# Kernel tuning notes

Measured on AMD Instinct MI355X. Metric: run time of the kernel, lower is better.

The kernel has to match this reference:

```python
import jax, jax.numpy as jnp
import numpy as np

K = 10

def _lrelu(v):
    return jax.nn.leaky_relu(v, negative_slope=0.2)

def _knn_idx(x, k):
    # x: [B, C, N]; returns indices of k nearest neighbors [B, N, k]
    xx = jnp.sum(x * x, axis=1, keepdims=True)          # [B,1,N]
    inner = -2.0 * jnp.einsum('bcn,bcm->bnm', x, x)     # [B,N,N]
    pd = -xx - inner - jnp.swapaxes(xx, 1, 2)           # -squared distance [B,N,N]
    _, idx = jax.lax.top_k(pd, k)
    return idx

def _graph_feature(x, k):
    # x: [B, C, N] -> edge features [B, 2C, N, k]
    idx = _knn_idx(x, k)                                # [B,N,k]
    xt = jnp.swapaxes(x, 1, 2)                          # [B,N,C]
    feat = jax.vmap(lambda xb, ib: xb[ib])(xt, idx)     # [B,N,k,C] gather
    center = xt[:, :, None, :]                          # [B,N,1,C]
    f = jnp.concatenate([feat - center,
                         jnp.broadcast_to(center, feat.shape)], axis=-1)  # [B,N,k,2C]
    return jnp.transpose(f, (0, 3, 1, 2))               # [B,2C,N,k]

def _edge_block(x, W, k):
    # conv2d 1x1 (no bias) + LeakyReLU + max over neighbors
    g = _graph_feature(x, k)                            # [B,2C,N,k]
    h = _lrelu(jnp.einsum('oc,bcnk->bonk', W, g))
    return jnp.max(h, axis=-1)                          # [B,O,N]

def setup_inputs() -> dict:
    key = jax.random.key(0)
    ks = jax.random.split(key, 9)
    def w(k_, *shape):
        fan_in = shape[-1]
        return jax.random.normal(k_, shape, dtype=jnp.float32) / np.sqrt(fan_in)
    return {
        'x':  jax.random.normal(ks[0], (8, 3, 2048), dtype=jnp.float32),
        'W1': w(ks[1], 64, 6),
        'W2': w(ks[2], 64, 128),
        'W3': w(ks[3], 128, 128),
        'W4': w(ks[4], 256, 256),
        'W5': w(ks[5], 512, 512),
        'L1': w(ks[6], 512, 1024),
        'L2': w(ks[7], 256, 512),
        'b2': jnp.zeros((256,), dtype=jnp.float32),
    }

def reference(x, W1, W2, W3, W4, W5, L1, L2, b2):
    x1 = _edge_block(x,  W1, K)   # [B,64,N]
    x2 = _edge_block(x1, W2, K)   # [B,64,N]
    x3 = _edge_block(x2, W3, K)   # [B,128,N]
    x4 = _edge_block(x3, W4, K)   # [B,256,N]
    h = jnp.concatenate([x1, x2, x3, x4], axis=1)        # [B,512,N]
    h = _lrelu(jnp.einsum('oc,bcn->bon', W5, h))         # [B,512,N]
    hmax = jnp.max(h, axis=-1)                           # [B,512]
    havg = jnp.mean(h, axis=-1)                          # [B,512]
    f = jnp.concatenate([hmax, havg], axis=1)            # [B,1024]
    f = _lrelu(f @ L1.T)                                 # [B,512]
    out = _lrelu(f @ L2.T + b2)                          # [B,256]
    return out
```

## Files before the change

### kernel.cpp

```cpp
#include <hip/hip_runtime.h>
#include <cstdint>
#include <cstddef>

constexpr int B_ = 8;
constexpr int N_ = 2048;
constexpr int K_ = 10;

typedef __attribute__((ext_vector_type(8))) short bf16x8;
typedef __attribute__((ext_vector_type(4))) float f32x4;

__device__ __forceinline__ float lrelu(float v) { return fmaxf(v, 0.2f * v); }

__device__ __forceinline__ short f2bf(float f) {
    uint32_t u = __builtin_bit_cast(uint32_t, f);
    u += 0x7fff + ((u >> 16) & 1);
    return (short)(u >> 16);
}
__device__ __forceinline__ float bf2f(short s) {
    uint32_t x = ((uint32_t)(unsigned short)s) << 16;
    return __builtin_bit_cast(float, x);
}

__global__ void k_transpose(const float* __restrict__ x, float* __restrict__ xt) {
    int i = blockIdx.x * 256 + threadIdx.x;
    if (i >= B_ * N_) return;
    int b = i / N_, n = i % N_;
#pragma unroll
    for (int c = 0; c < 3; ++c)
        xt[(size_t)i * 3 + c] = x[((size_t)b * 3 + c) * N_ + n];
}

__global__ void k_cvt(const float* __restrict__ W4, const float* __restrict__ W5,
                      short* __restrict__ Wb4, short* __restrict__ W5b) {
    int i = blockIdx.x * 256 + threadIdx.x;
    if (i < 256 * 128) {
        Wb4[i] = f2bf(W4[(size_t)(i >> 7) * 256 + (i & 127)]);
    } else {
        int k = i - 256 * 128;
        if (k < 512 * 512) W5b[k] = f2bf(W5[k]);
    }
}

__global__ void k_cvt2(const float* __restrict__ W2, const float* __restrict__ W3,
                       short* __restrict__ w2h, short* __restrict__ w2l,
                       short* __restrict__ w3h, short* __restrict__ w3l) {
    int i = blockIdx.x * 256 + threadIdx.x;
    if (i < 64 * 64) {
        float v = W2[(size_t)(i >> 6) * 128 + (i & 63)];
        short h = f2bf(v);
        w2h[i] = h; w2l[i] = f2bf(v - bf2f(h));
    } else if (i < 64 * 64 + 128 * 64) {
        int k = i - 64 * 64;
        float v = W3[(size_t)(k >> 6) * 128 + (k & 63)];
        short h = f2bf(v);
        w3h[k] = h; w3l[k] = f2bf(v - bf2f(h));
    }
}

template <int C>
__global__ __launch_bounds__(256) void k_cvthl(const float* __restrict__ hcat, int OFF,
                                               unsigned short* __restrict__ xhi,
                                               unsigned short* __restrict__ xlo) {
    int i = blockIdx.x * 256 + threadIdx.x;
    if (i >= B_ * N_ * C / 4) return;
    int row = i / (C / 4), q = i % (C / 4);
    const float4 v = *(const float4*)&hcat[(size_t)row * 512 + OFF + q * 4];
    float a4[4] = {v.x, v.y, v.z, v.w};
    short h4[4], l4[4];
#pragma unroll
    for (int e = 0; e < 4; ++e) {
        h4[e] = f2bf(a4[e]);
        l4[e] = f2bf(a4[e] - bf2f(h4[e]));
    }
    *(short4*)&xhi[(size_t)i * 4] = make_short4(h4[0], h4[1], h4[2], h4[3]);
    *(short4*)&xlo[(size_t)i * 4] = make_short4(l4[0], l4[1], l4[2], l4[3]);
}

__global__ void k_norms(const float* __restrict__ xt, int LD, int OFF, int C,
                        float* __restrict__ nrm) {
    int gid = blockIdx.x * 256 + threadIdx.x;
    int wid = gid >> 6;
    int lane = threadIdx.x & 63;
    if (wid >= B_ * N_) return;
    const float* row = xt + (size_t)wid * LD + OFF;
    float s = 0.f;
    for (int c = lane; c < C; c += 64) { float v = row[c]; s += v * v; }
#pragma unroll
    for (int off = 32; off; off >>= 1) s += __shfl_down(s, off);
    if (lane == 0) nrm[wid] = s;
}

__global__ __launch_bounds__(256) void k_knn3(const float* __restrict__ x,
                                              int* __restrict__ idxout) {
    __shared__ float xs[3][N_];
    __shared__ float ns[N_];
    const int b = blockIdx.x;
    const int w = threadIdx.x >> 6, lane = threadIdx.x & 63;
    const int n = blockIdx.y * 4 + w;
    for (int e = threadIdx.x; e < 3 * N_; e += 256)
        xs[e / N_][e % N_] = x[(size_t)b * 3 * N_ + e];
    __syncthreads();
    for (int m = threadIdx.x; m < N_; m += 256) {
        float a0 = xs[0][m], a1 = xs[1][m], a2 = xs[2][m];
        ns[m] = a0 * a0 + a1 * a1 + a2 * a2;
    }
    __syncthreads();
    const float q0 = xs[0][n], q1 = xs[1][n], q2 = xs[2][n];

    float sv[32];
#pragma unroll
    for (int g = 0; g < 32; ++g) {
        int m = g * 64 + lane;
        sv[g] = 2.f * (q0 * xs[0][m] + q1 * xs[1][m] + q2 * xs[2][m]) - ns[m];
    }
    float lm = sv[0];
#pragma unroll
    for (int g = 1; g < 32; ++g) lm = fmaxf(lm, sv[g]);
    float cur = lm, T = lm;
#pragma unroll
    for (int i = 0; i < K_; ++i) {
        float wm = cur;
#pragma unroll
        for (int off = 1; off < 64; off <<= 1) wm = fmaxf(wm, __shfl_xor(wm, off));
        T = wm;
        unsigned long long m = __ballot(cur == wm);
        int first = __ffsll(m) - 1;
        if (lane == first) cur = -INFINITY;
    }
    float kv[K_]; int ki[K_];
#pragma unroll
    for (int i = 0; i < K_; ++i) { kv[i] = -INFINITY; ki[i] = 0x7fffffff; }
#pragma unroll
    for (int g = 0; g < 32; ++g) {
        unsigned long long mk = __ballot(sv[g] >= T && sv[g] > kv[0]);
        while (mk) {
            int l = __ffsll(mk) - 1;
            mk &= mk - 1;
            float v = __shfl(sv[g], l);
            if (v > kv[0]) {
                kv[0] = v; ki[0] = g * 64 + l;
#pragma unroll
                for (int u = 0; u < K_ - 1; ++u)
                    if (kv[u] > kv[u + 1]) {
                        float tv = kv[u]; kv[u] = kv[u + 1]; kv[u + 1] = tv;
                        int tix = ki[u]; ki[u] = ki[u + 1]; ki[u + 1] = tix;
                    }
            }
        }
    }
    if (lane == 0) {
        int* op = idxout + ((size_t)b * N_ + n) * K_;
#pragma unroll
        for (int k = 0; k < K_; ++k) op[k] = ki[K_ - 1 - k];
    }
}

template <int C>
__global__ __launch_bounds__(256) void k_scores_mfma(const unsigned short* __restrict__ xhi,
                                                     const unsigned short* __restrict__ xlo,
                                                     const float* __restrict__ nrm,
                                                     float* __restrict__ S, int b0) {
    constexpr int RPC = C / 64;
    constexpr int NCH = 3 * RPC;
    constexpr int T = N_ / 64;
    __shared__ short AN[64 * 64];
    __shared__ short AM[64 * 64];
    const int bl = blockIdx.x;
    const int b = b0 + bl;
    int p = blockIdx.y;
    int r0 = 0, off = 0;
    while (off + (T - r0) <= p) { off += T - r0; ++r0; }
    const int ti = r0, tj = r0 + (p - off);
    const int n0 = ti * 64, m0 = tj * 64;
    const int t = threadIdx.x;
    const int lane = t & 63, w = t >> 6;
    const int colg = lane & 15, kg = lane >> 4;
    const size_t bbase = (size_t)b * N_;
    const float* nb = nrm + bbase;
    float* Sb = S + (size_t)bl * N_ * N_;

    f32x4 acc[4];
#pragma unroll
    for (int j = 0; j < 4; ++j) acc[j] = (f32x4){0.f, 0.f, 0.f, 0.f};

    for (int ch = 0; ch < NCH; ++ch) {
        const int region = ch / RPC;
        const int cc0 = (ch % RPC) * 64;
        const unsigned short* an_src = (region == 1) ? xlo : xhi;
        const unsigned short* am_src = (region == 2) ? xlo : xhi;
        __syncthreads();
#pragma unroll
        for (int e = 0; e < 2; ++e) {
            int idx = t + e * 256;
            int r = idx >> 3, k8 = idx & 7;
            uint4 vn = *(const uint4*)&an_src[(bbase + n0 + r) * C + cc0 + k8 * 8];
            uint4 vm = *(const uint4*)&am_src[(bbase + m0 + r) * C + cc0 + k8 * 8];
            int byte = (r * 128 + k8 * 16) ^ ((r & 7) << 4);
            *(uint4*)((char*)AN + byte) = vn;
            *(uint4*)((char*)AM + byte) = vm;
        }
        __syncthreads();
        const int arow = w * 16 + colg;
#pragma unroll
        for (int s = 0; s < 2; ++s) {
            int abyte = (arow * 128 + s * 64 + kg * 16) ^ ((arow & 7) << 4);
            bf16x8 af = *(const bf16x8*)((const char*)AN + abyte);
#pragma unroll
            for (int j = 0; j < 4; ++j) {
                int brow = j * 16 + colg;
                int bbyte = (brow * 128 + s * 64 + kg * 16) ^ ((brow & 7) << 4);
                bf16x8 bfr = *(const bf16x8*)((const char*)AM + bbyte);
                acc[j] = __builtin_amdgcn_mfma_f32_16x16x32_bf16(af, bfr, acc[j], 0, 0, 0);
            }
        }
    }
#pragma unroll
    for (int j = 0; j < 4; ++j) {
        float nm = nb[m0 + j * 16 + colg];
#pragma unroll
        for (int r = 0; r < 4; ++r) {
            int row = n0 + w * 16 + kg * 4 + r;
            Sb[(size_t)row * N_ + m0 + j * 16 + colg] = 2.f * acc[j][r] - nm;
        }
    }
    if (ti != tj) {
#pragma unroll
        for (int r = 0; r < 4; ++r) {
            int nrow = n0 + w * 16 + kg * 4 + r;
            float nn = nb[nrow];
#pragma unroll
            for (int j = 0; j < 4; ++j)
                Sb[(size_t)(m0 + j * 16 + colg) * N_ + nrow] = 2.f * acc[j][r] - nn;
        }
    }
}

__global__ __launch_bounds__(256) void k_topk(const float* __restrict__ S,
                                              int* __restrict__ idxout, int b0) {
    const int bl = blockIdx.x, b = b0 + bl;
    const int wv = threadIdx.x >> 6, lane = threadIdx.x & 63;
    const int n = blockIdx.y * 4 + wv;
    const float* row = S + (size_t)bl * N_ * N_ + (size_t)n * N_;

    float sv[32];
#pragma unroll
    for (int g = 0; g < 32; ++g) sv[g] = __builtin_nontemporal_load(&row[g * 64 + lane]);

    float lm = sv[0];
#pragma unroll
    for (int g = 1; g < 32; ++g) lm = fmaxf(lm, sv[g]);

    float cur = lm, T = lm;
#pragma unroll
    for (int i = 0; i < K_; ++i) {
        float wm = cur;
#pragma unroll
        for (int off = 1; off < 64; off <<= 1) wm = fmaxf(wm, __shfl_xor(wm, off));
        T = wm;
        unsigned long long m = __ballot(cur == wm);
        int first = __ffsll(m) - 1;
        if (lane == first) cur = -INFINITY;
    }

    float kv[K_]; int ki[K_];
#pragma unroll
    for (int i = 0; i < K_; ++i) { kv[i] = -INFINITY; ki[i] = 0x7fffffff; }

#pragma unroll
    for (int g = 0; g < 32; ++g) {
        unsigned long long mk = __ballot(sv[g] >= T && sv[g] > kv[0]);
        while (mk) {
            int l = __ffsll(mk) - 1;
            mk &= mk - 1;
            float v = __shfl(sv[g], l);
            if (v > kv[0]) {
                kv[0] = v; ki[0] = g * 64 + l;
#pragma unroll
                for (int u = 0; u < K_ - 1; ++u)
                    if (kv[u] > kv[u + 1]) {
                        float tv = kv[u]; kv[u] = kv[u + 1]; kv[u + 1] = tv;
                        int tix = ki[u]; ki[u] = ki[u + 1]; ki[u + 1] = tix;
                    }
            }
        }
    }
    if (lane == 0) {
        int* op = idxout + ((size_t)b * N_ + n) * K_;
#pragma unroll
        for (int k = 0; k < K_; ++k) op[k] = ki[K_ - 1 - k];
    }
}

template <int C, int O>
__global__ __launch_bounds__(256) void k_center(const float* __restrict__ xt, int LD, int OFF,
                                                const float* __restrict__ W,
                                                float* __restrict__ tbuf) {
    constexpr int KC = (C == 3) ? 4 : 32;
    __shared__ __align__(16) float XT[64][36];
    __shared__ __align__(16) float WDT[KC][68];
    const int b = blockIdx.x;
    const int n0 = blockIdx.y * 64;
    const int ob = blockIdx.z * 64;
    const int t = threadIdx.x;
    const int tn = t & 15, to = t >> 4;
    const float* xb = xt + ((size_t)b * N_) * LD + OFF;
    float4 acc[4];
#pragma unroll
    for (int i = 0; i < 4; ++i) acc[i] = make_float4(0, 0, 0, 0);
    for (int c0 = 0; c0 < C; c0 += KC) {
        __syncthreads();
        for (int e = t; e < 64 * KC; e += 256) {
            int r = e / KC, cc = e % KC;
            XT[r][cc] = (C == 3) ? ((cc < 3) ? xb[(size_t)(n0 + r) * LD + cc] : 0.f)
                                 : xb[(size_t)(n0 + r) * LD + c0 + cc];
        }
        for (int e = t; e < 64 * KC; e += 256) {
            int oo = e / KC, cc = e % KC;
            float wd, wc;
            if (C == 3) {
                wd = (cc < 3) ? W[(ob + oo) * 6 + cc] : 0.f;
                wc = (cc < 3) ? W[(ob + oo) * 6 + 3 + cc] : 0.f;
            } else {
                wd = W[(size_t)(ob + oo) * (2 * C) + c0 + cc];
                wc = W[(size_t)(ob + oo) * (2 * C) + C + c0 + cc];
            }
            WDT[cc][oo] = wc - wd;
        }
        __syncthreads();
#pragma unroll 4
        for (int cc = 0; cc < KC; ++cc) {
            float4 w4 = *(const float4*)&WDT[cc][to * 4];
#pragma unroll
            for (int i = 0; i < 4; ++i) {
                float a = XT[tn * 4 + i][cc];
                acc[i].x += a * w4.x; acc[i].y += a * w4.y;
                acc[i].z += a * w4.z; acc[i].w += a * w4.w;
            }
        }
    }
#pragma unroll
    for (int i = 0; i < 4; ++i)
        *(float4*)&tbuf[((size_t)b * N_ + n0 + tn * 4 + i) * O + ob + to * 4] = acc[i];
}

template <int C, int O>
__global__ __launch_bounds__(256) void k_conv(const float* __restrict__ xt, int LDI, int OFFI,
                                              const int* __restrict__ idx,
                                              const float* __restrict__ W,
                                              const float* __restrict__ tbuf,
                                              float* __restrict__ hout, int OFFO) {
    constexpr int KC = (C == 3) ? 4 : 32;
    __shared__ __align__(16) float A[160][36];
    __shared__ __align__(16) float WT[KC][68];
    __shared__ int nb_s[160];
    const int b = blockIdx.x;
    const int n0 = blockIdx.y * 16;
    const int t = threadIdx.x;
    const int p = t >> 4, og = t & 15;
    if (t < 160) nb_s[t] = idx[((size_t)b * N_ + n0 + t / K_) * K_ + (t % K_)];
    const float* xb = xt + ((size_t)b * N_) * LDI + OFFI;

    for (int ob = 0; ob < O; ob += 64) {
        float4 acc[K_];
#pragma unroll
        for (int j = 0; j < K_; ++j) acc[j] = make_float4(0, 0, 0, 0);
        for (int c0 = 0; c0 < C; c0 += KC) {
            __syncthreads();
            if (C == 3) {
                for (int e = t; e < 160 * 4; e += 256) {
                    int r = e / 4, cc = e % 4;
                    A[r][cc] = (cc < 3) ? xb[(size_t)nb_s[r] * LDI + cc] : 0.f;
                }
            } else {
                for (int e = t; e < 160 * 8; e += 256) {
                    int r = e / 8, c4 = e % 8;
                    *(float4*)&A[r][c4 * 4] =
                        *(const float4*)&xb[(size_t)nb_s[r] * LDI + c0 + c4 * 4];
                }
            }
            for (int e = t; e < 64 * KC; e += 256) {
                int oo = e / KC, cc = e % KC;
                float w;
                if (C == 3) w = (cc < 3) ? W[(ob + oo) * 6 + cc] : 0.f;
                else        w = W[(size_t)(ob + oo) * (2 * C) + c0 + cc];
                WT[cc][oo] = w;
            }
            __syncthreads();
#pragma unroll 4
            for (int cc = 0; cc < KC; ++cc) {
                float4 w4 = *(const float4*)&WT[cc][og * 4];
#pragma unroll
                for (int j = 0; j < K_; ++j) {
                    float a = A[p * K_ + j][cc];
                    acc[j].x += a * w4.x; acc[j].y += a * w4.y;
                    acc[j].z += a * w4.z; acc[j].w += a * w4.w;
                }
            }
        }
        float4 tv = *(const float4*)&tbuf[((size_t)b * N_ + n0 + p) * O + ob + og * 4];
        float4 mx = acc[0];
#pragma unroll
        for (int j = 1; j < K_; ++j) {
            mx.x = fmaxf(mx.x, acc[j].x); mx.y = fmaxf(mx.y, acc[j].y);
            mx.z = fmaxf(mx.z, acc[j].z); mx.w = fmaxf(mx.w, acc[j].w);
        }
        float4 r;
        r.x = lrelu(mx.x + tv.x); r.y = lrelu(mx.y + tv.y);
        r.z = lrelu(mx.z + tv.z); r.w = lrelu(mx.w + tv.w);
        *(float4*)&hout[((size_t)b * N_ + n0 + p) * 512 + OFFO + ob + og * 4] = r;
    }
}

template <int O>
__global__ __launch_bounds__(256) void k_conv23_mfma(const float* __restrict__ hcat, int OFFI,
                                                     const int* __restrict__ idx,
                                                     const short* __restrict__ Wh,
                                                     const short* __restrict__ Wl,
                                                     const float* __restrict__ tbuf,
                                                     float* __restrict__ hout, int OFFO) {
    constexpr int CT = O / 64;
    __shared__ short Ah[160 * 64];
    __shared__ short Al[160 * 64];
    __shared__ int nb_s[160];
    const int b = blockIdx.x;
    const int n0 = blockIdx.y * 16;
    const int t = threadIdx.x;
    const int lane = t & 63, wv = t >> 6;
    const int colg = lane & 15, kg = lane >> 4;
    if (t < 160) nb_s[t] = idx[((size_t)b * N_ + n0 + t / K_) * K_ + (t % K_)];
    __syncthreads();
    for (int e = t; e < 160 * 16; e += 256) {
        int r = e >> 4, q = e & 15;
        const float4 v = *(const float4*)&hcat[((size_t)b * N_ + nb_s[r]) * 512 + OFFI + q * 4];
        float a4[4] = {v.x, v.y, v.z, v.w};
        short sh[4], sl[4];
#pragma unroll
        for (int c2 = 0; c2 < 4; ++c2) {
            sh[c2] = f2bf(a4[c2]);
            sl[c2] = f2bf(a4[c2] - bf2f(sh[c2]));
        }
        int byte = r * 128 + ((q * 8) ^ (((r / K_) & 7) << 4));
        *(short4*)((char*)Ah + byte) = make_short4(sh[0], sh[1], sh[2], sh[3]);
        *(short4*)((char*)Al + byte) = make_short4(sl[0], sl[1], sl[2], sl[3]);
    }
    bf16x8 bh[CT][2], blo[CT][2];
    const int obase = wv * (O / 4);
#pragma unroll
    for (int ct = 0; ct < CT; ++ct)
#pragma unroll
        for (int ks = 0; ks < 2; ++ks) {
            int o = obase + ct * 16 + colg;
            bh[ct][ks]  = *(const bf16x8*)&Wh[(size_t)o * 64 + ks * 32 + kg * 8];
            blo[ct][ks] = *(const bf16x8*)&Wl[(size_t)o * 64 + ks * 32 + kg * 8];
        }
    __syncthreads();

    f32x4 macc[CT];
#pragma unroll
    for (int ct = 0; ct < CT; ++ct)
        macc[ct] = (f32x4){-INFINITY, -INFINITY, -INFINITY, -INFINITY};

    const int aswz = (colg & 7) << 4;
#pragma unroll
    for (int j = 0; j < K_; ++j) {
        const int arow = colg * K_ + j;
        bf16x8 afh[2], afl[2];
#pragma unroll
        for (int ks = 0; ks < 2; ++ks) {
            int byte = arow * 128 + ((ks * 64 + kg * 16) ^ aswz);
            afh[ks] = *(const bf16x8*)((const char*)Ah + byte);
            afl[ks] = *(const bf16x8*)((const char*)Al + byte);
        }
        f32x4 acc[CT];
#pragma unroll
        for (int ct = 0; ct < CT; ++ct) acc[ct] = (f32x4){0.f, 0.f, 0.f, 0.f};
#pragma unroll
        for (int ks = 0; ks < 2; ++ks)
#pragma unroll
            for (int ct = 0; ct < CT; ++ct)
                acc[ct] = __builtin_amdgcn_mfma_f32_16x16x32_bf16(afh[ks], bh[ct][ks], acc[ct], 0, 0, 0);
#pragma unroll
        for (int ks = 0; ks < 2; ++ks)
#pragma unroll
            for (int ct = 0; ct < CT; ++ct)
                acc[ct] = __builtin_amdgcn_mfma_f32_16x16x32_bf16(afl[ks], bh[ct][ks], acc[ct], 0, 0, 0);
#pragma unroll
        for (int ks = 0; ks < 2; ++ks)
#pragma unroll
            for (int ct = 0; ct < CT; ++ct)
                acc[ct] = __builtin_amdgcn_mfma_f32_16x16x32_bf16(afh[ks], blo[ct][ks], acc[ct], 0, 0, 0);
#pragma unroll
        for (int ct = 0; ct < CT; ++ct) {
            macc[ct].x = fmaxf(macc[ct].x, acc[ct].x);
            macc[ct].y = fmaxf(macc[ct].y, acc[ct].y);
            macc[ct].z = fmaxf(macc[ct].z, acc[ct].z);
            macc[ct].w = fmaxf(macc[ct].w, acc[ct].w);
        }
    }
#pragma unroll
    for (int ct = 0; ct < CT; ++ct)
#pragma unroll
        for (int r = 0; r < 4; ++r) {
            int p = kg * 4 + r;
            int o = obase + ct * 16 + colg;
            float v = macc[ct][r] + tbuf[((size_t)b * N_ + n0 + p) * O + o];
            hout[((size_t)b * N_ + n0 + p) * 512 + OFFO + o] = lrelu(v);
        }
}

__global__ __launch_bounds__(256) void k_conv4_mfma(const float* __restrict__ hcat,
                                                    const int* __restrict__ idx,
                                                    const short* __restrict__ Wb,
                                                    const float* __restrict__ tbuf,
                                                    float* __restrict__ hout) {
    __shared__ short Ab[160 * 128];
    __shared__ int nb_s[160];
    const int b = blockIdx.x;
    const int n0 = blockIdx.y * 16;
    const int t = threadIdx.x;
    const int lane = t & 63, wv = t >> 6;
    const int colg = lane & 15, kg = lane >> 4;
    if (t < 160) nb_s[t] = idx[((size_t)b * N_ + n0 + t / K_) * K_ + (t % K_)];
    __syncthreads();
    for (int e = t; e < 160 * 32; e += 256) {
        int r = e >> 5, q = e & 31;
        const float4 v = *(const float4*)&hcat[((size_t)b * N_ + nb_s[r]) * 512 + 128 + q * 4];
        short4 s4 = { f2bf(v.x), f2bf(v.y), f2bf(v.z), f2bf(v.w) };
        int byte = r * 256 + ((q * 8) ^ (((r / K_) & 7) << 4));
        *(short4*)((char*)Ab + byte) = s4;
    }
    bf16x8 bf[4][4];
    const int ob = wv * 64;
#pragma unroll
    for (int nt = 0; nt < 4; ++nt)
#pragma unroll
        for (int ks = 0; ks < 4; ++ks)
            bf[nt][ks] = *(const bf16x8*)&Wb[(size_t)(ob + nt * 16 + colg) * 128 + ks * 32 + kg * 8];
    __syncthreads();

    f32x4 macc[4];
#pragma unroll
    for (int nt = 0; nt < 4; ++nt)
        macc[nt] = (f32x4){-INFINITY, -INFINITY, -INFINITY, -INFINITY};

    const int arow = colg * K_;
    const int aswz = (colg & 7) << 4;
#pragma unroll
    for (int j = 0; j < K_; ++j) {
        f32x4 acc[4];
#pragma unroll
        for (int nt = 0; nt < 4; ++nt) acc[nt] = (f32x4){0.f, 0.f, 0.f, 0.f};
#pragma unroll
        for (int ks = 0; ks < 4; ++ks) {
            int byte = (arow + j) * 256 + (((ks * 32 + kg * 8) * 2) ^ aswz);
            bf16x8 af = *(const bf16x8*)((const char*)Ab + byte);
#pragma unroll
            for (int nt = 0; nt < 4; ++nt)
                acc[nt] = __builtin_amdgcn_mfma_f32_16x16x32_bf16(af, bf[nt][ks], acc[nt], 0, 0, 0);
        }
#pragma unroll
        for (int nt = 0; nt < 4; ++nt) {
            macc[nt].x = fmaxf(macc[nt].x, acc[nt].x);
            macc[nt].y = fmaxf(macc[nt].y, acc[nt].y);
            macc[nt].z = fmaxf(macc[nt].z, acc[nt].z);
            macc[nt].w = fmaxf(macc[nt].w, acc[nt].w);
        }
    }
#pragma unroll
    for (int nt = 0; nt < 4; ++nt)
#pragma unroll
        for (int r = 0; r < 4; ++r) {
            int p = kg * 4 + r;
            int o = ob + nt * 16 + colg;
            float v = macc[nt][r] + tbuf[((size_t)b * N_ + n0 + p) * 256 + o];
            hout[((size_t)b * N_ + n0 + p) * 512 + 256 + o] = lrelu(v);
        }
}

__global__ __launch_bounds__(256) void k_final_mfma(const float* __restrict__ hcat,
                                                    const short* __restrict__ W5b,
                                                    float* __restrict__ pmax,
                                                    float* __restrict__ psum) {
    __shared__ short Ab[64 * 128];
    const int b = blockIdx.x, nc = blockIdx.y, obk = blockIdx.z;
    const int n0 = nc * 64, ob = obk * 64;
    const int t = threadIdx.x, lane = t & 63, wv = t >> 6;
    const int colg = lane & 15, kg = lane >> 4;
    const int o = ob + wv * 16 + colg;

    f32x4 acc[4];
#pragma unroll
    for (int mt = 0; mt < 4; ++mt) acc[mt] = (f32x4){0.f, 0.f, 0.f, 0.f};

    for (int kc = 0; kc < 4; ++kc) {
        __syncthreads();
        for (int e = t; e < 64 * 32; e += 256) {
            int r = e >> 5, q = e & 31;
            const float4 v = *(const float4*)&hcat[((size_t)b * N_ + n0 + r) * 512 + kc * 128 + q * 4];
            short4 s4 = { f2bf(v.x), f2bf(v.y), f2bf(v.z), f2bf(v.w) };
            int byte = r * 256 + ((q * 8) ^ ((r & 7) << 4));
            *(short4*)((char*)Ab + byte) = s4;
        }
        __syncthreads();
#pragma unroll
        for (int ks = 0; ks < 4; ++ks) {
            bf16x8 bfrag = *(const bf16x8*)&W5b[(size_t)o * 512 + kc * 128 + ks * 32 + kg * 8];
#pragma unroll
            for (int mt = 0; mt < 4; ++mt) {
                int row = mt * 16 + colg;
                int byte = row * 256 + (((ks * 32 + kg * 8) * 2) ^ ((row & 7) << 4));
                bf16x8 af = *(const bf16x8*)((const char*)Ab + byte);
                acc[mt] = __builtin_amdgcn_mfma_f32_16x16x32_bf16(af, bfrag, acc[mt], 0, 0, 0);
            }
        }
    }
    float mx = -INFINITY, sm = 0.f;
#pragma unroll
    for (int mt = 0; mt < 4; ++mt)
#pragma unroll
        for (int r = 0; r < 4; ++r) {
            float v = lrelu(acc[mt][r]);
            mx = fmaxf(mx, v); sm += v;
        }
    mx = fmaxf(mx, __shfl_xor(mx, 16)); sm += __shfl_xor(sm, 16);
    mx = fmaxf(mx, __shfl_xor(mx, 32)); sm += __shfl_xor(sm, 32);
    if (lane < 16) {
        pmax[((size_t)b * 512 + ob + wv * 16 + lane) * 32 + nc] = mx;
        psum[((size_t)b * 512 + ob + wv * 16 + lane) * 32 + nc] = sm;
    }
}

__global__ __launch_bounds__(256) void k_pool(const float* __restrict__ pmax,
                                              const float* __restrict__ psum,
                                              float* __restrict__ f) {
    int i = blockIdx.x * 256 + threadIdx.x;
    if (i >= B_ * 512) return;
    int b = i >> 9, o = i & 511;
    const float* pm = pmax + (size_t)i * 32;
    const float* ps = psum + (size_t)i * 32;
    float mm = -INFINITY, ss = 0.f;
#pragma unroll
    for (int q = 0; q < 32; ++q) { mm = fmaxf(mm, pm[q]); ss += ps[q]; }
    f[(size_t)b * 1024 + o] = mm;
    f[(size_t)b * 1024 + 512 + o] = ss * (1.0f / 2048.0f);
}

__global__ __launch_bounds__(256) void k_fc1(const float* __restrict__ f,
                                             const float* __restrict__ L1,
                                             float* __restrict__ f1) {
    __shared__ float fs[8][1024];
    const int t = threadIdx.x, lane = t & 63, w = t >> 6;
    for (int e = t; e < 2048; e += 256)
        *(float4*)&fs[0][e * 4] = *(const float4*)&f[e * 4];
    __syncthreads();
    const int o = blockIdx.x * 4 + w;
    float acc[8];
#pragma unroll
    for (int b = 0; b < 8; ++b) acc[b] = 0.f;
    const float* Lrow = L1 + (size_t)o * 1024;
#pragma unroll
    for (int e = 0; e < 16; ++e) {
        float wv = Lrow[e * 64 + lane];
#pragma unroll
        for (int b = 0; b < 8; ++b) acc[b] += wv * fs[b][e * 64 + lane];
    }
#pragma unroll
    for (int off = 32; off; off >>= 1)
#pragma unroll
        for (int b = 0; b < 8; ++b) acc[b] += __shfl_xor(acc[b], off);
#pragma unroll
    for (int b = 0; b < 8; ++b)
        if (lane == b) f1[(size_t)b * 512 + o] = lrelu(acc[b]);
}

__global__ __launch_bounds__(256) void k_fc2(const float* __restrict__ f1,
                                             const float* __restrict__ L2,
                                             const float* __restrict__ b2,
                                             float* __restrict__ out) {
    __shared__ float fs[8][512];
    const int t = threadIdx.x, lane = t & 63, w = t >> 6;
    for (int e = t; e < 1024; e += 256)
        *(float4*)&fs[0][e * 4] = *(const float4*)&f1[e * 4];
    __syncthreads();
    const int o = blockIdx.x * 4 + w;
    float acc[8];
#pragma unroll
    for (int b = 0; b < 8; ++b) acc[b] = 0.f;
    const float* Lrow = L2 + (size_t)o * 512;
#pragma unroll
    for (int e = 0; e < 8; ++e) {
        float wv = Lrow[e * 64 + lane];
#pragma unroll
        for (int b = 0; b < 8; ++b) acc[b] += wv * fs[b][e * 64 + lane];
    }
#pragma unroll
    for (int off = 32; off; off >>= 1)
#pragma unroll
        for (int b = 0; b < 8; ++b) acc[b] += __shfl_xor(acc[b], off);
    float bb = b2[o];
#pragma unroll
    for (int b = 0; b < 8; ++b)
        if (lane == b) out[(size_t)b * 256 + o] = lrelu(acc[b] + bb);
}

extern "C" void kernel_launch(void* const* d_in, const int* in_sizes, int n_in,
                              void* d_out, int out_size, void* d_ws, size_t ws_size,
                              hipStream_t stream) {
    (void)in_sizes; (void)n_in; (void)out_size;
    const float* x  = (const float*)d_in[0];
    const float* W1 = (const float*)d_in[1];
    const float* W2 = (const float*)d_in[2];
    const float* W3 = (const float*)d_in[3];
    const float* W4 = (const float*)d_in[4];
    const float* W5 = (const float*)d_in[5];
    const float* L1 = (const float*)d_in[6];
    const float* L2 = (const float*)d_in[7];
    const float* b2 = (const float*)d_in[8];
    float* out = (float*)d_out;

    float* ws   = (float*)d_ws;
    float* xt   = ws;
    float* nrm  = xt + (size_t)B_ * N_ * 3;
    int*   idxb = (int*)(nrm + (size_t)B_ * N_);
    float* tb   = (float*)(idxb + (size_t)B_ * N_ * K_);
    float* hcat = tb + (size_t)B_ * N_ * 256;
    float* pmax = hcat + (size_t)B_ * N_ * 512;
    float* psum = pmax + (size_t)B_ * 512 * 32;
    short* wb4  = (short*)(psum + (size_t)B_ * 512 * 32);
    short* w5b  = wb4 + 256 * 128;
    short* w2h  = w5b + 512 * 512;
    short* w2l  = w2h + 64 * 64;
    short* w3h  = w2l + 64 * 64;
    short* w3l  = w3h + 128 * 64;
    float* fbuf = (float*)(w3l + 128 * 64);
    float* f1b  = fbuf + 8192;
    unsigned short* xh = (unsigned short*)(f1b + 4096);
    unsigned short* xl = xh + (size_t)B_ * N_ * 128;
    float* scor = (float*)(xl + (size_t)B_ * N_ * 128);

    const size_t base_f = 49152 + 16384 + 163840 + 4194304 + 8388608 +
                          131072 + 131072 + 16384 + 131072 + 12288 + 8192 + 4096 +
                          2097152;
    const size_t nsq = (size_t)N_ * N_;
    size_t avail = (ws_size / 4 > base_f) ? (ws_size / 4 - base_f) : 0;
    int CH = 1;
    if (avail >= 8 * nsq) CH = 8;
    else if (avail >= 4 * nsq) CH = 4;
    else if (avail >= 2 * nsq) CH = 2;

    constexpr int TP = (N_ / 64) * (N_ / 64 + 1) / 2;

    dim3 blk(256);
    k_transpose<<<dim3((B_ * N_ + 255) / 256), blk, 0, stream>>>(x, xt);
    k_cvt<<<dim3((256 * 128 + 512 * 512 + 255) / 256), blk, 0, stream>>>(W4, W5, wb4, w5b);
    k_cvt2<<<dim3((64 * 64 + 128 * 64 + 255) / 256), blk, 0, stream>>>(W2, W3, w2h, w2l, w3h, w3l);

    k_knn3<<<dim3(B_, N_ / 4), blk, 0, stream>>>(x, idxb);
    k_center<3, 64><<<dim3(B_, N_ / 64, 1), blk, 0, stream>>>(xt, 3, 0, W1, tb);
    k_conv<3, 64><<<dim3(B_, N_ / 16), blk, 0, stream>>>(xt, 3, 0, idxb, W1, tb, hcat, 0);

    k_norms<<<dim3(B_ * N_ / 4), blk, 0, stream>>>(hcat, 512, 0, 64, nrm);
    k_cvthl<64><<<dim3(B_ * N_ * 64 / 4 / 256), blk, 0, stream>>>(hcat, 0, xh, xl);
    for (int b0 = 0; b0 < B_; b0 += CH) {
        k_scores_mfma<64><<<dim3(CH, TP), blk, 0, stream>>>(xh, xl, nrm, scor, b0);
        k_topk<<<dim3(CH, N_ / 4), blk, 0, stream>>>(scor, idxb, b0);
    }
    k_center<64, 64><<<dim3(B_, N_ / 64, 1), blk, 0, stream>>>(hcat, 512, 0, W2, tb);
    k_conv23_mfma<64><<<dim3(B_, N_ / 16), blk, 0, stream>>>(hcat, 0, idxb, w2h, w2l, tb, hcat, 64);

    k_norms<<<dim3(B_ * N_ / 4), blk, 0, stream>>>(hcat, 512, 64, 64, nrm);
    k_cvthl<64><<<dim3(B_ * N_ * 64 / 4 / 256), blk, 0, stream>>>(hcat, 64, xh, xl);
    for (int b0 = 0; b0 < B_; b0 += CH) {
        k_scores_mfma<64><<<dim3(CH, TP), blk, 0, stream>>>(xh, xl, nrm, scor, b0);
        k_topk<<<dim3(CH, N_ / 4), blk, 0, stream>>>(scor, idxb, b0);
    }
    k_center<64, 128><<<dim3(B_, N_ / 64, 2), blk, 0, stream>>>(hcat, 512, 64, W3, tb);
    k_conv23_mfma<128><<<dim3(B_, N_ / 16), blk, 0, stream>>>(hcat, 64, idxb, w3h, w3l, tb, hcat, 128);

    k_norms<<<dim3(B_ * N_ / 4), blk, 0, stream>>>(hcat, 512, 128, 128, nrm);
    k_cvthl<128><<<dim3(B_ * N_ * 128 / 4 / 256), blk, 0, stream>>>(hcat, 128, xh, xl);
    for (int b0 = 0; b0 < B_; b0 += CH) {
        k_scores_mfma<128><<<dim3(CH, TP), blk, 0, stream>>>(xh, xl, nrm, scor, b0);
        k_topk<<<dim3(CH, N_ / 4), blk, 0, stream>>>(scor, idxb, b0);
    }
    k_center<128, 256><<<dim3(B_, N_ / 64, 4), blk, 0, stream>>>(hcat, 512, 128, W4, tb);
    k_conv4_mfma<<<dim3(B_, N_ / 16), blk, 0, stream>>>(hcat, idxb, wb4, tb, hcat);

    k_final_mfma<<<dim3(B_, 32, 8), blk, 0, stream>>>(hcat, w5b, pmax, psum);
    k_pool<<<dim3(B_ * 512 / 256), blk, 0, stream>>>(pmax, psum, fbuf);
    k_fc1<<<dim3(128), blk, 0, stream>>>(fbuf, L1, f1b);
    k_fc2<<<dim3(64), blk, 0, stream>>>(f1b, L2, b2, out);
}
```

Baseline: 464.8 us.

## Split first-layer kNN across column chunks with merge; fuse norms and bf16 split

The first-layer kNN kernel is split along the candidate dimension into two column chunks. Each chunk produces a partial top-k of values and indices, and a new merge kernel combines them with tie-breaking on the lower index. This doubles the block count and halves the per-block shared memory and register arrays, which should improve occupancy for that stage at the cost of an extra launch and a small amount of scratch traffic. Separately, the row-norm and hi/lo bf16 conversion kernels are fused into one pass per layer, so each activation row is read once and one launch per layer goes away.

```diff
diff --git a/kernel.cpp b/kernel.cpp
--- a/kernel.cpp
+++ b/kernel.cpp
@@ -58,64 +58,67 @@
 }
 
 template <int C>
-__global__ __launch_bounds__(256) void k_cvthl(const float* __restrict__ hcat, int OFF,
-                                               unsigned short* __restrict__ xhi,
-                                               unsigned short* __restrict__ xlo) {
-    int i = blockIdx.x * 256 + threadIdx.x;
-    if (i >= B_ * N_ * C / 4) return;
-    int row = i / (C / 4), q = i % (C / 4);
-    const float4 v = *(const float4*)&hcat[(size_t)row * 512 + OFF + q * 4];
-    float a4[4] = {v.x, v.y, v.z, v.w};
-    short h4[4], l4[4];
-#pragma unroll
-    for (int e = 0; e < 4; ++e) {
-        h4[e] = f2bf(a4[e]);
-        l4[e] = f2bf(a4[e] - bf2f(h4[e]));
-    }
-    *(short4*)&xhi[(size_t)i * 4] = make_short4(h4[0], h4[1], h4[2], h4[3]);
-    *(short4*)&xlo[(size_t)i * 4] = make_short4(l4[0], l4[1], l4[2], l4[3]);
-}
-
-__global__ void k_norms(const float* __restrict__ xt, int LD, int OFF, int C,
-                        float* __restrict__ nrm) {
+__global__ __launch_bounds__(256) void k_prep(const float* __restrict__ hcat, int OFF,
+                                              unsigned short* __restrict__ xhi,
+                                              unsigned short* __restrict__ xlo,
+                                              float* __restrict__ nrm) {
     int gid = blockIdx.x * 256 + threadIdx.x;
     int wid = gid >> 6;
     int lane = threadIdx.x & 63;
     if (wid >= B_ * N_) return;
-    const float* row = xt + (size_t)wid * LD + OFF;
-    float s = 0.f;
-    for (int c = lane; c < C; c += 64) { float v = row[c]; s += v * v; }
+    const float* row = hcat + (size_t)wid * 512 + OFF;
+    float v0 = row[lane];
+    short h0 = f2bf(v0);
+    xhi[(size_t)wid * C + lane] = (unsigned short)h0;
+    xlo[(size_t)wid * C + lane] = (unsigned short)f2bf(v0 - bf2f(h0));
+    float s = v0 * v0;
+    if (C == 128) {
+        float v1 = row[64 + lane];
+        short h1 = f2bf(v1);
+        xhi[(size_t)wid * C + 64 + lane] = (unsigned short)h1;
+        xlo[(size_t)wid * C + 64 + lane] = (unsigned short)f2bf(v1 - bf2f(h1));
+        s += v1 * v1;
+    }
 #pragma unroll
     for (int off = 32; off; off >>= 1) s += __shfl_down(s, off);
     if (lane == 0) nrm[wid] = s;
 }
 
-__global__ __launch_bounds__(256) void k_knn3(const float* __restrict__ x,
-                                              int* __restrict__ idxout) {
-    __shared__ float xs[3][N_];
-    __shared__ float ns[N_];
+template <int CS>
+__global__ __launch_bounds__(256) void k_knn3p(const float* __restrict__ x,
+                                               float* __restrict__ pv, int* __restrict__ pi) {
+    constexpr int COLS = N_ / CS;
+    constexpr int NG = COLS / 64;
+    __shared__ float xs[3][COLS];
+    __shared__ float ns[COLS];
     const int b = blockIdx.x;
     const int w = threadIdx.x >> 6, lane = threadIdx.x & 63;
     const int n = blockIdx.y * 4 + w;
-    for (int e = threadIdx.x; e < 3 * N_; e += 256)
-        xs[e / N_][e % N_] = x[(size_t)b * 3 * N_ + e];
+    const int cs = blockIdx.z;
+    const int mbase = cs * COLS;
+    for (int e = threadIdx.x; e < 3 * COLS; e += 256) {
+        int c = e / COLS, mm = e % COLS;
+        xs[c][mm] = x[((size_t)b * 3 + c) * N_ + mbase + mm];
+    }
     __syncthreads();
-    for (int m = threadIdx.x; m < N_; m += 256) {
+    for (int m = threadIdx.x; m < COLS; m += 256) {
         float a0 = xs[0][m], a1 = xs[1][m], a2 = xs[2][m];
         ns[m] = a0 * a0 + a1 * a1 + a2 * a2;
     }
     __syncthreads();
-    const float q0 = xs[0][n], q1 = xs[1][n], q2 = xs[2][n];
-
-    float sv[32];
-#pragma unroll
-    for (int g = 0; g < 32; ++g) {
+    const float q0 = x[((size_t)b * 3 + 0) * N_ + n];
+    const float q1 = x[((size_t)b * 3 + 1) * N_ + n];
+    const float q2 = x[((size_t)b * 3 + 2) * N_ + n];
+
+    float sv[NG];
+#pragma unroll
+    for (int g = 0; g < NG; ++g) {
         int m = g * 64 + lane;
         sv[g] = 2.f * (q0 * xs[0][m] + q1 * xs[1][m] + q2 * xs[2][m]) - ns[m];
     }
     float lm = sv[0];
 #pragma unroll
-    for (int g = 1; g < 32; ++g) lm = fmaxf(lm, sv[g]);
+    for (int g = 1; g < NG; ++g) lm = fmaxf(lm, sv[g]);
     float cur = lm, T = lm;
 #pragma unroll
     for (int i = 0; i < K_; ++i) {
@@ -131,14 +134,14 @@
 #pragma unroll
     for (int i = 0; i < K_; ++i) { kv[i] = -INFINITY; ki[i] = 0x7fffffff; }
 #pragma unroll
-    for (int g = 0; g < 32; ++g) {
+    for (int g = 0; g < NG; ++g) {
         unsigned long long mk = __ballot(sv[g] >= T && sv[g] > kv[0]);
         while (mk) {
             int l = __ffsll(mk) - 1;
             mk &= mk - 1;
             float v = __shfl(sv[g], l);
             if (v > kv[0]) {
-                kv[0] = v; ki[0] = g * 64 + l;
+                kv[0] = v; ki[0] = mbase + g * 64 + l;
 #pragma unroll
                 for (int u = 0; u < K_ - 1; ++u)
                     if (kv[u] > kv[u + 1]) {
@@ -149,9 +152,35 @@
         }
     }
     if (lane == 0) {
-        int* op = idxout + ((size_t)b * N_ + n) * K_;
-#pragma unroll
-        for (int k = 0; k < K_; ++k) op[k] = ki[K_ - 1 - k];
+        float* opv = pv + (((size_t)b * N_ + n) * CS + cs) * K_;
+        int*   opi = pi + (((size_t)b * N_ + n) * CS + cs) * K_;
+#pragma unroll
+        for (int k = 0; k < K_; ++k) { opv[k] = kv[K_ - 1 - k]; opi[k] = ki[K_ - 1 - k]; }
+    }
+}
+
+template <int CS>
+__global__ __launch_bounds__(256) void k_kmerge(const float* __restrict__ pv,
+                                                const int* __restrict__ pi,
+                                                int* __restrict__ idxout) {
+    int row = blockIdx.x * 256 + threadIdx.x;
+    if (row >= B_ * N_) return;
+    const float* rv = pv + (size_t)row * CS * K_;
+    const int*   ri = pi + (size_t)row * CS * K_;
+    int p[CS];
+#pragma unroll
+    for (int q = 0; q < CS; ++q) p[q] = 0;
+    int* op = idxout + (size_t)row * K_;
+    for (int k = 0; k < K_; ++k) {
+        float bv = -INFINITY; int bi = 0x7fffffff, bq = 0;
+#pragma unroll
+        for (int q = 0; q < CS; ++q) {
+            float v = rv[q * K_ + p[q]];
+            int id = ri[q * K_ + p[q]];
+            if (v > bv || (v == bv && id < bi)) { bv = v; bi = id; bq = q; }
+        }
+        op[k] = bi;
+        ++p[bq];
     }
 }
 
@@ -718,6 +747,8 @@
     const float* b2 = (const float*)d_in[8];
     float* out = (float*)d_out;
 
+    constexpr int CS = 2;
+
     float* ws   = (float*)d_ws;
     float* xt   = ws;
     float* nrm  = xt + (size_t)B_ * N_ * 3;
@@ -736,11 +767,13 @@
     float* f1b  = fbuf + 8192;
     unsigned short* xh = (unsigned short*)(f1b + 4096);
     unsigned short* xl = xh + (size_t)B_ * N_ * 128;
-    float* scor = (float*)(xl + (size_t)B_ * N_ * 128);
+    float* pv   = (float*)(xl + (size_t)B_ * N_ * 128);
+    int*   pi   = (int*)(pv + (size_t)B_ * N_ * CS * K_);
+    float* scor = (float*)(pi + (size_t)B_ * N_ * CS * K_);
 
     const size_t base_f = 49152 + 16384 + 163840 + 4194304 + 8388608 +
                           131072 + 131072 + 16384 + 131072 + 12288 + 8192 + 4096 +
-                          2097152;
+                          2097152 + 655360;
     const size_t nsq = (size_t)N_ * N_;
     size_t avail = (ws_size / 4 > base_f) ? (ws_size / 4 - base_f) : 0;
     int CH = 1;
@@ -755,12 +788,12 @@
     k_cvt<<<dim3((256 * 128 + 512 * 512 + 255) / 256), blk, 0, stream>>>(W4, W5, wb4, w5b);
     k_cvt2<<<dim3((64 * 64 + 128 * 64 + 255) / 256), blk, 0, stream>>>(W2, W3, w2h, w2l, w3h, w3l);
 
-    k_knn3<<<dim3(B_, N_ / 4), blk, 0, stream>>>(x, idxb);
+    k_knn3p<CS><<<dim3(B_, N_ / 4, CS), blk, 0, stream>>>(x, pv, pi);
+    k_kmerge<CS><<<dim3(B_ * N_ / 256), blk, 0, stream>>>(pv, pi, idxb);
     k_center<3, 64><<<dim3(B_, N_ / 64, 1), blk, 0, stream>>>(xt, 3, 0, W1, tb);
     k_conv<3, 64><<<dim3(B_, N_ / 16), blk, 0, stream>>>(xt, 3, 0, idxb, W1, tb, hcat, 0);
 
-    k_norms<<<dim3(B_ * N_ / 4), blk, 0, stream>>>(hcat, 512, 0, 64, nrm);
-    k_cvthl<64><<<dim3(B_ * N_ * 64 / 4 / 256), blk, 0, stream>>>(hcat, 0, xh, xl);
+    k_prep<64><<<dim3(B_ * N_ / 4), blk, 0, stream>>>(hcat, 0, xh, xl, nrm);
     for (int b0 = 0; b0 < B_; b0 += CH) {
         k_scores_mfma<64><<<dim3(CH, TP), blk, 0, stream>>>(xh, xl, nrm, scor, b0);
         k_topk<<<dim3(CH, N_ / 4), blk, 0, stream>>>(scor, idxb, b0);
@@ -768,8 +801,7 @@
     k_center<64, 64><<<dim3(B_, N_ / 64, 1), blk, 0, stream>>>(hcat, 512, 0, W2, tb);
     k_conv23_mfma<64><<<dim3(B_, N_ / 16), blk, 0, stream>>>(hcat, 0, idxb, w2h, w2l, tb, hcat, 64);
 
-    k_norms<<<dim3(B_ * N_ / 4), blk, 0, stream>>>(hcat, 512, 64, 64, nrm);
-    k_cvthl<64><<<dim3(B_ * N_ * 64 / 4 / 256), blk, 0, stream>>>(hcat, 64, xh, xl);
+    k_prep<64><<<dim3(B_ * N_ / 4), blk, 0, stream>>>(hcat, 64, xh, xl, nrm);
     for (int b0 = 0; b0 < B_; b0 += CH) {
         k_scores_mfma<64><<<dim3(CH, TP), blk, 0, stream>>>(xh, xl, nrm, scor, b0);
         k_topk<<<dim3(CH, N_ / 4), blk, 0, stream>>>(scor, idxb, b0);
@@ -777,8 +809,7 @@
     k_center<64, 128><<<dim3(B_, N_ / 64, 2), blk, 0, stream>>>(hcat, 512, 64, W3, tb);
     k_conv23_mfma<128><<<dim3(B_, N_ / 16), blk, 0, stream>>>(hcat, 64, idxb, w3h, w3l, tb, hcat, 128);
 
-    k_norms<<<dim3(B_ * N_ / 4), blk, 0, stream>>>(hcat, 512, 128, 128, nrm);
-    k_cvthl<128><<<dim3(B_ * N_ * 128 / 4 / 256), blk, 0, stream>>>(hcat, 128, xh, xl);
+    k_prep<128><<<dim3(B_ * N_ / 4), blk, 0, stream>>>(hcat, 128, xh, xl, nrm);
     for (int b0 = 0; b0 < B_; b0 += CH) {
         k_scores_mfma<128><<<dim3(CH, TP), blk, 0, stream>>>(xh, xl, nrm, scor, b0);
         k_topk<<<dim3(CH, N_ / 4), blk, 0, stream>>>(scor, idxb, b0);
```

Measured after the change: 486.2 us. 1.05x slower.
